# Kernel optimization log

Hardware: AMD Instinct MI355X
Metric: run time of the kernel (lower is better)

The kernel has to match this reference:

```python
import jax, jax.numpy as jnp
import numpy as np

N_HEADS = 16
LN_EPS = 1e-5

def _layernorm(x, g, b):
    m = jnp.mean(x, axis=-1, keepdims=True)
    v = jnp.var(x, axis=-1, keepdims=True)
    return (x - m) * jax.lax.rsqrt(v + LN_EPS) * g + b

def setup_inputs() -> dict:
    key = jax.random.key(0)
    ks = jax.random.split(key, 6)
    B, L, D = 4, 1024, 1024
    Dff = 4 * D
    s = 0.02  # init scale to keep logits/activations in a sane range
    return {
        "X": jax.random.normal(ks[0], (B, L, D), jnp.float32),
        "wq": jax.random.normal(ks[1], (D, D), jnp.float32) * s,
        "wk": jax.random.normal(ks[2], (D, D), jnp.float32) * s,
        "wv": jax.random.normal(ks[3], (D, D), jnp.float32) * s,
        "ln1_g": jnp.ones((D,), jnp.float32),
        "ln1_b": jnp.zeros((D,), jnp.float32),
        "w1": jax.random.normal(ks[4], (Dff, D), jnp.float32) * s,
        "b1": jnp.zeros((Dff,), jnp.float32),
        "w2": jax.random.normal(ks[5], (D, Dff), jnp.float32) * s,
        "b2": jnp.zeros((D,), jnp.float32),
        "ln2_g": jnp.ones((D,), jnp.float32),
        "ln2_b": jnp.zeros((D,), jnp.float32),
    }

def reference(X, wq, wk, wv, ln1_g, ln1_b, w1, b1, w2, b2, ln2_g, ln2_b):
    B, L, D = X.shape
    H = N_HEADS
    dh = D // H
    # qkv projections (torch Linear: x @ W^T), split into heads
    Q = (X @ wq.T).reshape(B, L, H, dh)
    K = (X @ wk.T).reshape(B, L, H, dh)
    V = (X @ wv.T).reshape(B, L, H, dh)
    scores = jnp.einsum("blhd,bmhd->bhlm", Q, K)  # [B,H,L,L]
    causal = jnp.tril(jnp.ones((L, L), dtype=bool))
    scores = jnp.where(causal, scores, -jnp.inf)
    attn = jax.nn.softmax(scores / jnp.sqrt(jnp.asarray(dh, X.dtype)), axis=-1)
    ctx = jnp.einsum("bhlm,bmhd->blhd", attn, V).reshape(B, L, D)
    # post-LN residual (note: no output projection after attention)
    X = _layernorm(X + ctx, ln1_g, ln1_b)
    h = jax.nn.selu(X @ w1.T + b1)
    X = _layernorm(X + h @ w2.T + b2, ln2_g, ln2_b)
    return X
```

## Files before the change

kernel.cpp:

```cpp
#include <hip/hip_runtime.h>
#include <hip/hip_bf16.h>

#define BATCH 4
#define SEQ   1024
#define DIM   1024
#define NH    16
#define DH    64
#define DFF   4096
#define MTOK  (BATCH*SEQ)

#define QSCALE 0.1803368801111204f

typedef __attribute__((ext_vector_type(8))) short  short8;
typedef __attribute__((ext_vector_type(4))) short  short4v;
typedef __attribute__((ext_vector_type(4))) float  floatx4;
typedef __attribute__((ext_vector_type(4))) float  float4v;
typedef __attribute__((ext_vector_type(4))) int    int4v;

__device__ inline float bf2f(short s) {
    return __uint_as_float(((unsigned int)(unsigned short)s) << 16);
}
__device__ inline short f2bf(float f) {
    __hip_bfloat16 h = __float2bfloat16(f);
    return *reinterpret_cast<short*>(&h);
}

__device__ inline float wave_sum(float v) {
    #pragma unroll
    for (int off = 32; off >= 1; off >>= 1) v += __shfl_xor(v, off);
    return v;
}

__device__ inline void async_ld16(short* lds, const short* g) {
    __builtin_amdgcn_global_load_lds(
        (const __attribute__((address_space(1))) void*)g,
        (__attribute__((address_space(3))) void*)lds, 16, 0, 0);
}

#define GBAR() do { asm volatile("" ::: "memory");            \
                    __builtin_amdgcn_s_barrier();             \
                    asm volatile("" ::: "memory"); } while (0)

__global__ __launch_bounds__(256) void convert_all(
    const float* __restrict__ sX,  short* __restrict__ dX,
    const float* __restrict__ sq,  short* __restrict__ dq,
    const float* __restrict__ sk,  short* __restrict__ dk,
    const float* __restrict__ sv,  short* __restrict__ dv,
    const float* __restrict__ s1,  short* __restrict__ d1,
    const float* __restrict__ s2,  short* __restrict__ d2)
{
    int cid = blockIdx.x * 256 + threadIdx.x;
    const float* src; short* dst; int base;
    if      (cid <  524288) { src = sX; dst = dX; base = 0; }
    else if (cid <  655360) { src = sq; dst = dq; base = 524288; }
    else if (cid <  786432) { src = sk; dst = dk; base = 655360; }
    else if (cid <  917504) { src = sv; dst = dv; base = 786432; }
    else if (cid < 1441792) { src = s1; dst = d1; base = 917504; }
    else                    { src = s2; dst = d2; base = 1441792; }
    size_t i = (size_t)(cid - base) * 8;
    float4v f0 = *(const float4v*)(src + i);
    float4v f1 = *(const float4v*)(src + i + 4);
    short8 o;
    o[0]=f2bf(f0[0]); o[1]=f2bf(f0[1]); o[2]=f2bf(f0[2]); o[3]=f2bf(f0[3]);
    o[4]=f2bf(f1[0]); o[5]=f2bf(f1[1]); o[6]=f2bf(f1[2]); o[7]=f2bf(f1[3]);
    *(short8*)(dst + i) = o;
}

template<int EPI>
__global__ __launch_bounds__(512, 2) void gemm256(
    const short* __restrict__ A, const short* __restrict__ B,
    const float* __restrict__ bias, short* __restrict__ C, int N, int K)
{
    __shared__ __align__(16) short Ls[65536];

    const int t    = threadIdx.x;
    const int lane = t & 63;
    const int wave = t >> 6;
    const int quad = lane >> 4;
    const int l15  = lane & 15;
    const int wm   = wave >> 2;
    const int wn   = wave & 3;

    const int nwg2 = gridDim.x * gridDim.y;
    const int lin  = blockIdx.y * gridDim.x + blockIdx.x;
    const int qch  = nwg2 >> 3;
    const int swzb = (lin & 7) * qch + (lin >> 3);
    const int tm   = (swzb % gridDim.x) * 256;
    const int tn   = (swzb / gridDim.x) * 256;

    int kbase = 0, klen = K;
    if (EPI == 3) { klen = K >> 2; kbase = blockIdx.z * klen; }
    const int NT = klen >> 6;

    const int r0 = t >> 3;
    const int rb = ((t >> 8) & 1) * 64 + ((t >> 3) & 31);
    const int g8 = (((t & 7) ^ ((t >> 3) & 7)) << 3);
    const int offAL[2] = { r0*K + g8,          (128 + r0)*K + g8 };
    const int offAH[2] = { (64 + r0)*K + g8,   (192 + r0)*K + g8 };
    const int offB0[2] = { rb*K + g8,          (128 + rb)*K + g8 };
    const int offB1[2] = { (32 + rb)*K + g8,   (160 + rb)*K + g8 };
    const short* Abase = A + (size_t)tm * K + kbase;
    const short* Bbase = B + (size_t)tn * K + kbase;
    short* dstb = &Ls[t * 8];

    const int xa  = (wm*64 + l15) * 64;
    const int xb  = (wn*32 + l15) * 64;
    const int sw  = l15 & 7;
    const int xc0 = ((quad ^ sw) << 3);
    const int xc1 = (((4 + quad) ^ sw) << 3);

    short8 a[4][2], b[4][2];
    floatx4 acc[8][4];
    #pragma unroll
    for (int mt = 0; mt < 8; mt++)
        #pragma unroll
        for (int nt = 0; nt < 4; nt++) acc[mt][nt] = {0.f, 0.f, 0.f, 0.f};

#define STAGE(buf, slot, offs, base, k0) do {                         \
        short* _d = dstb + (buf)*32768 + (slot)*8192;                 \
        async_ld16(_d,        (base) + (offs)[0] + (k0));             \
        async_ld16(_d + 4096, (base) + (offs)[1] + (k0));             \
    } while (0)

#define LDA4(buf, hf) do { _Pragma("unroll")                          \
    for (int _mt = 0; _mt < 4; _mt++) {                               \
        a[_mt][0] = *(const short8*)&Ls[(buf)*32768 + (hf)*8192 + xa + _mt*1024 + xc0]; \
        a[_mt][1] = *(const short8*)&Ls[(buf)*32768 + (hf)*8192 + xa + _mt*1024 + xc1]; \
    } } while (0)

#define LDB2(buf, bh, o) do { _Pragma("unroll")                       \
    for (int _nn = 0; _nn < 2; _nn++) {                               \
        b[(o)+_nn][0] = *(const short8*)&Ls[(buf)*32768 + 16384 + (bh)*8192 + xb + _nn*1024 + xc0]; \
        b[(o)+_nn][1] = *(const short8*)&Ls[(buf)*32768 + 16384 + (bh)*8192 + xb + _nn*1024 + xc1]; \
    } } while (0)

#define MM8(mb, nb) do { __builtin_amdgcn_s_setprio(1); _Pragma("unroll") \
    for (int _mt = 0; _mt < 4; _mt++) { _Pragma("unroll")             \
        for (int _nn = 0; _nn < 2; _nn++) {                           \
            acc[(mb)+_mt][(nb)+_nn] = __builtin_amdgcn_mfma_f32_16x16x32_bf16( \
                a[_mt][0], b[(nb)+_nn][0], acc[(mb)+_mt][(nb)+_nn], 0, 0, 0);  \
            acc[(mb)+_mt][(nb)+_nn] = __builtin_amdgcn_mfma_f32_16x16x32_bf16( \
                a[_mt][1], b[(nb)+_nn][1], acc[(mb)+_mt][(nb)+_nn], 0, 0, 0);  \
        } }                                                           \
    __builtin_amdgcn_s_setprio(0); } while (0)

    STAGE(0, 0, offAL, Abase, 0);
    STAGE(0, 2, offB0, Bbase, 0);
    STAGE(0, 3, offB1, Bbase, 0);
    STAGE(0, 1, offAH, Abase, 0);
    asm volatile("s_waitcnt vmcnt(4)" ::: "memory");
    STAGE(1, 0, offAL, Abase, 64);
    STAGE(1, 2, offB0, Bbase, 64);
    STAGE(1, 3, offB1, Bbase, 64);
    asm volatile("s_waitcnt vmcnt(6)" ::: "memory");
    GBAR();

    for (int kt = 0; kt < NT; ++kt) {
        const int  cur = (kt & 1), nxt = cur ^ 1;
        const bool s1  = (kt + 1 < NT);
        const bool s2  = (kt + 2 < NT);
        const int  k1  = (kt + 1) << 6;
        const int  k2  = (kt + 2) << 6;
        LDA4(cur, 0);
        LDB2(cur, 0, 0);
        if (s1) STAGE(nxt, 1, offAH, Abase, k1);
        asm volatile("s_waitcnt lgkmcnt(8)" ::: "memory");
        GBAR(); MM8(0, 0); GBAR();
        LDB2(cur, 1, 2);
        if (s2) STAGE(cur, 0, offAL, Abase, k2);
        GBAR(); MM8(0, 2); GBAR();
        LDA4(cur, 1);
        if (s2) STAGE(cur, 2, offB0, Bbase, k2);
        GBAR(); MM8(4, 0); GBAR();
        if (s2) STAGE(cur, 3, offB1, Bbase, k2);
        if (kt == NT - 2)
            asm volatile("s_waitcnt vmcnt(0)" ::: "memory");
        else if (kt < NT - 2)
            asm volatile("s_waitcnt vmcnt(6)" ::: "memory");
        GBAR(); MM8(4, 2); GBAR();
    }

    const float SS = 1.0507009873554805f;
    const float SA = 1.6732632423543772f;

    #pragma unroll
    for (int mt = 0; mt < 8; mt++) {
        int row0 = tm + wm*128 + (mt >> 2)*64 + (mt & 3)*16 + quad*4;
        #pragma unroll
        for (int nt = 0; nt < 4; nt++) {
            int col = tn + wn*64 + nt*16 + l15;
            if (EPI == 0 && (col >> 10) == 2) {
                int h = (col >> 6) & 15, d = col & 63;
                int bb = row0 >> 10, key = row0 & 1023;
                short4v pv;
                #pragma unroll
                for (int r = 0; r < 4; r++) pv[r] = f2bf(acc[mt][nt][r]);
                *(short4v*)&C[(size_t)2*MTOK*1024
                    + ((size_t)(bb*16 + h)*64 + d)*1024 + key] = pv;
                continue;
            }
            #pragma unroll
            for (int r = 0; r < 4; r++) {
                int row = row0 + r;
                float v = acc[mt][nt][r];
                if (EPI == 0) {
                    int which = col >> 10;
                    if (which == 0) v *= QSCALE;
                    C[(size_t)which * ((size_t)MTOK*1024)
                      + (size_t)row * 1024 + (col & 1023)] = f2bf(v);
                } else if (EPI == 1) {
                    v += bias[col];
                    v = (v > 0.f) ? SS * v
                                  : SS * SA * (exp2f(v * 1.44269504f) - 1.f);
                    C[(size_t)row * N + col] = f2bf(v);
                } else {
                    C[(size_t)blockIdx.z * ((size_t)MTOK*N)
                      + (size_t)row * N + col] = f2bf(v);
                }
            }
        }
    }
#undef STAGE
#undef LDA4
#undef LDB2
#undef MM8
}

__global__ __launch_bounds__(256) void attn_kernel(
    const short* __restrict__ Q, const short* __restrict__ K,
    const short* __restrict__ Vt, short* __restrict__ CTX)
{
    __shared__ __align__(16) short Ks[2][64*64];
    __shared__ __align__(16) short Vs[2][64*64];
    __shared__ __align__(16) short Pl[4][32][72];

    const int t    = threadIdx.x;
    const int lane = t & 63;
    const int wave = t >> 6;
    const int quad = lane >> 4;
    const int l15  = lane & 15;
    const int q0 = (gridDim.x - 1 - blockIdx.x) * 128;
    const int bh = blockIdx.y;
    const int b  = bh >> 4;
    const int h  = bh & 15;

    const size_t headoff = (size_t)b * SEQ * DIM + (size_t)h * DH;
    const short* Qb  = Q + headoff;
    const short* Kb  = K + headoff;
    const short* Vtb = Vt + (size_t)bh * DH * SEQ;

    const int wrow0 = q0 + wave*32;

    short8 aq[2][2];
    #pragma unroll
    for (int mg = 0; mg < 2; mg++)
        #pragma unroll
        for (int c = 0; c < 2; c++)
            aq[mg][c] = *(const short8*)(Qb
                + (size_t)(wrow0 + mg*16 + l15) * DIM + c*32 + quad*8);

    short8 bones;
    {
        short v = (l15 == 0) ? (short)0x3F80 : (short)0;
        #pragma unroll
        for (int e = 0; e < 8; e++) bones[e] = v;
    }

    floatx4 o[2][4], ol[2];
    #pragma unroll
    for (int mg = 0; mg < 2; mg++) {
        #pragma unroll
        for (int nt = 0; nt < 4; nt++) o[mg][nt] = {0.f, 0.f, 0.f, 0.f};
        ol[mg] = {0.f, 0.f, 0.f, 0.f};
    }

    const int swz = (((t & 7) ^ ((t >> 3) & 7))) * 8;
    auto stage = [&](int j0, int sb) {
        #pragma unroll
        for (int p = 0; p < 2; p++) {
            async_ld16(Ks[sb] + (t + p*256)*8,
                       Kb + (size_t)(j0 + (t>>3) + p*32) * DIM + swz);
            async_ld16(Vs[sb] + (t + p*256)*8,
                       Vtb + (size_t)((t>>3) + p*32) * SEQ + j0 + swz);
        }
    };

    const int jend = q0 + 128;
    stage(0, 0);
    __syncthreads();

    int sb = 0;
    for (int j0 = 0; j0 < jend; j0 += 64) {
        if (j0 + 64 < jend) stage(j0 + 64, sb ^ 1);

        if (j0 <= wrow0 + 31) {
            floatx4 s[2][4];
            #pragma unroll
            for (int mg = 0; mg < 2; mg++)
                #pragma unroll
                for (int nt = 0; nt < 4; nt++) s[mg][nt] = {0.f, 0.f, 0.f, 0.f};
            #pragma unroll
            for (int c = 0; c < 2; c++) {
                #pragma unroll
                for (int nt = 0; nt < 4; nt++) {
                    short8 bk = *(const short8*)&Ks[sb][(nt*16 + l15)*64
                                  + ((c*4 + quad) ^ (l15 & 7))*8];
                    s[0][nt] = __builtin_amdgcn_mfma_f32_16x16x32_bf16(bk, aq[0][c], s[0][nt], 0, 0, 0);
                    s[1][nt] = __builtin_amdgcn_mfma_f32_16x16x32_bf16(bk, aq[1][c], s[1][nt], 0, 0, 0);
                }
            }

            if (j0 + 63 > wrow0) {
                #pragma unroll
                for (int mg = 0; mg < 2; mg++) {
                    int rowq = wrow0 + mg*16 + l15;
                    #pragma unroll
                    for (int nt = 0; nt < 4; nt++) {
                        #pragma unroll
                        for (int r = 0; r < 4; r++) {
                            int key = j0 + nt*16 + quad*4 + r;
                            if (key > rowq) s[mg][nt][r] = -1.0e38f;
                        }
                    }
                }
            }

            #pragma unroll
            for (int mg = 0; mg < 2; mg++)
                #pragma unroll
                for (int nt = 0; nt < 4; nt++) {
                    short4v pv;
                    #pragma unroll
                    for (int r = 0; r < 4; r++)
                        pv[r] = f2bf(exp2f(s[mg][nt][r]));
                    *(short4v*)&Pl[wave][mg*16 + l15][nt*16 + quad*4] = pv;
                }

            #pragma unroll
            for (int c = 0; c < 2; c++) {
                short8 ap0 = *(const short8*)&Pl[wave][l15][c*32 + quad*8];
                short8 ap1 = *(const short8*)&Pl[wave][16 + l15][c*32 + quad*8];
                #pragma unroll
                for (int nt = 0; nt < 4; nt++) {
                    short8 bv = *(const short8*)&Vs[sb][(nt*16 + l15)*64
                                  + ((c*4 + quad) ^ (l15 & 7))*8];
                    o[0][nt] = __builtin_amdgcn_mfma_f32_16x16x32_bf16(ap0, bv, o[0][nt], 0, 0, 0);
                    o[1][nt] = __builtin_amdgcn_mfma_f32_16x16x32_bf16(ap1, bv, o[1][nt], 0, 0, 0);
                }
                ol[0] = __builtin_amdgcn_mfma_f32_16x16x32_bf16(ap0, bones, ol[0], 0, 0, 0);
                ol[1] = __builtin_amdgcn_mfma_f32_16x16x32_bf16(ap1, bones, ol[1], 0, 0, 0);
            }
        }

        __syncthreads();
        sb ^= 1;
    }

    #pragma unroll
    for (int mg = 0; mg < 2; mg++) {
        float linv[4];
        #pragma unroll
        for (int r = 0; r < 4; r++)
            linv[r] = 1.f / __shfl(ol[mg][r], lane & 48);
        #pragma unroll
        for (int nt = 0; nt < 4; nt++) {
            #pragma unroll
            for (int r = 0; r < 4; r++) {
                int rowq = wrow0 + mg*16 + quad*4 + r;
                int d    = nt*16 + l15;
                CTX[(size_t)b * SEQ * DIM + (size_t)rowq * DIM + h*DH + d]
                    = f2bf(o[mg][nt][r] * linv[r]);
            }
        }
    }
}

__global__ __launch_bounds__(256) void ln1_kernel(
    const float* __restrict__ X, const short* __restrict__ ctx,
    const float* __restrict__ g, const float* __restrict__ bvec,
    short* __restrict__ out)
{
    __shared__ float red[8];
    const size_t base = (size_t)blockIdx.x * DIM;
    const int wave = threadIdx.x >> 6;

    float x[4];
    float sum = 0.f, sq = 0.f;
    #pragma unroll
    for (int i = 0; i < 4; i++) {
        int idx = threadIdx.x + i*256;
        float v = X[base + idx] + bf2f(ctx[base + idx]);
        x[i] = v; sum += v; sq += v*v;
    }
    sum = wave_sum(sum); sq = wave_sum(sq);
    if ((threadIdx.x & 63) == 0) { red[wave] = sum; red[4 + wave] = sq; }
    __syncthreads();
    float s1 = red[0] + red[1] + red[2] + red[3];
    float s2 = red[4] + red[5] + red[6] + red[7];
    float mean = s1 * (1.f / DIM);
    float var  = s2 * (1.f / DIM) - mean * mean;
    float rstd = rsqrtf(var + 1e-5f);
    #pragma unroll
    for (int i = 0; i < 4; i++) {
        int idx = threadIdx.x + i*256;
        out[base + idx] = f2bf((x[i] - mean) * rstd * g[idx] + bvec[idx]);
    }
}

__global__ __launch_bounds__(256) void ln2_fused(
    const short* __restrict__ P, const float* __restrict__ bias,
    const short* __restrict__ x1, const float* __restrict__ g,
    const float* __restrict__ bvec, float* __restrict__ out)
{
    __shared__ float red[8];
    const size_t base = (size_t)blockIdx.x * DIM;
    const size_t E4 = (size_t)MTOK * 1024;
    const int wave = threadIdx.x >> 6;

    float x[4];
    float sum = 0.f, sq = 0.f;
    #pragma unroll
    for (int i = 0; i < 4; i++) {
        int idx = threadIdx.x + i*256;
        size_t p = base + idx;
        float v = bf2f(P[p]) + bf2f(P[E4 + p]) + bf2f(P[2*E4 + p])
                + bf2f(P[3*E4 + p]) + bias[idx] + bf2f(x1[p]);
        x[i] = v; sum += v; sq += v*v;
    }
    sum = wave_sum(sum); sq = wave_sum(sq);
    if ((threadIdx.x & 63) == 0) { red[wave] = sum; red[4 + wave] = sq; }
    __syncthreads();
    float s1 = red[0] + red[1] + red[2] + red[3];
    float s2 = red[4] + red[5] + red[6] + red[7];
    float mean = s1 * (1.f / DIM);
    float var  = s2 * (1.f / DIM) - mean * mean;
    float rstd = rsqrtf(var + 1e-5f);
    #pragma unroll
    for (int i = 0; i < 4; i++) {
        int idx = threadIdx.x + i*256;
        out[base + idx] = (x[i] - mean) * rstd * g[idx] + bvec[idx];
    }
}

extern "C" void kernel_launch(void* const* d_in, const int* in_sizes, int n_in,
                              void* d_out, int out_size, void* d_ws, size_t ws_size,
                              hipStream_t stream)
{
    const float* X   = (const float*)d_in[0];
    const float* wq  = (const float*)d_in[1];
    const float* wk  = (const float*)d_in[2];
    const float* wv  = (const float*)d_in[3];
    const float* g1  = (const float*)d_in[4];
    const float* b1  = (const float*)d_in[5];
    const float* w1  = (const float*)d_in[6];
    const float* bb1 = (const float*)d_in[7];
    const float* w2  = (const float*)d_in[8];
    const float* bb2 = (const float*)d_in[9];
    const float* g2  = (const float*)d_in[10];
    const float* b2  = (const float*)d_in[11];

    short* ws = (short*)d_ws;
    const size_t E1 = 1048576, E4 = 4194304;
    size_t o = 0;
    short* Xb    = ws + o; o += E4;
    short* wqkvb = ws + o; o += 3*E1;
    short* w1b   = ws + o; o += E4;
    short* w2b   = ws + o; o += E4;
    short* Q     = ws + o; o += E4;
    short* Kb    = ws + o; o += E4;
    short* Vt    = ws + o; o += E4;
    short* CTX   = ws + o; o += E4;
    short* X1    = ws + o; o += E4;
    short* P     = ws + o; o += 4*E4;
    short* Hf    = Q;

    dim3 blk(256);
    convert_all<<<dim3(7680), blk, 0, stream>>>(
        X, Xb, wq, wqkvb, wk, wqkvb + E1, wv, wqkvb + 2*E1,
        w1, w1b, w2, w2b);

    gemm256<0><<<dim3(MTOK/256, 3072/256), dim3(512), 0, stream>>>(
        Xb, wqkvb, nullptr, Q, 3072, DIM);
    attn_kernel<<<dim3(SEQ/128, BATCH*NH), blk, 0, stream>>>(Q, Kb, Vt, CTX);
    ln1_kernel<<<dim3(MTOK), blk, 0, stream>>>(X, CTX, g1, b1, X1);
    gemm256<1><<<dim3(MTOK/256, DFF/256), dim3(512), 0, stream>>>(
        X1, w1b, bb1, Hf, DFF, DIM);
    gemm256<3><<<dim3(MTOK/256, DIM/256, 4), dim3(512), 0, stream>>>(
        Hf, w2b, nullptr, P, DIM, DFF);
    ln2_fused<<<dim3(MTOK), blk, 0, stream>>>(P, bb2, X1, g2, b2, (float*)d_out);
}
```

Measured before the change: 290.7 us.

## Restructure GEMM main loop into two coarse phases and drop block swizzle

The bf16 GEMM inner loop is reorganised. Each iteration now loads all B fragments at once and runs two large MFMA batches (32 MFMAs each) separated by single barriers, instead of four interleaved load/compute/barrier sub-phases. The vmcnt waits are adjusted to match the new staging order. The XCD-aware block-index swizzle is replaced with plain blockIdx mapping. The aim is fewer barriers and waits, at the cost of less fine-grained overlap of LDS reads with MFMA and possibly worse L2 locality across XCDs.

After: 282.5 us. -2.8%, faster.

```diff
diff --git a/kernel.cpp b/kernel.cpp
--- a/kernel.cpp
+++ b/kernel.cpp
@@ -80,13 +80,8 @@
     const int l15  = lane & 15;
     const int wm   = wave >> 2;
     const int wn   = wave & 3;
-
-    const int nwg2 = gridDim.x * gridDim.y;
-    const int lin  = blockIdx.y * gridDim.x + blockIdx.x;
-    const int qch  = nwg2 >> 3;
-    const int swzb = (lin & 7) * qch + (lin >> 3);
-    const int tm   = (swzb % gridDim.x) * 256;
-    const int tn   = (swzb / gridDim.x) * 256;
+    const int tm   = blockIdx.x * 256;
+    const int tn   = blockIdx.y * 256;
 
     int kbase = 0, klen = K;
     if (EPI == 3) { klen = K >> 2; kbase = blockIdx.z * klen; }
@@ -128,56 +123,54 @@
         a[_mt][1] = *(const short8*)&Ls[(buf)*32768 + (hf)*8192 + xa + _mt*1024 + xc1]; \
     } } while (0)
 
-#define LDB2(buf, bh, o) do { _Pragma("unroll")                       \
-    for (int _nn = 0; _nn < 2; _nn++) {                               \
-        b[(o)+_nn][0] = *(const short8*)&Ls[(buf)*32768 + 16384 + (bh)*8192 + xb + _nn*1024 + xc0]; \
-        b[(o)+_nn][1] = *(const short8*)&Ls[(buf)*32768 + 16384 + (bh)*8192 + xb + _nn*1024 + xc1]; \
-    } } while (0)
-
-#define MM8(mb, nb) do { __builtin_amdgcn_s_setprio(1); _Pragma("unroll") \
-    for (int _mt = 0; _mt < 4; _mt++) { _Pragma("unroll")             \
+#define LDB4(buf) do { _Pragma("unroll")                              \
+    for (int _bh = 0; _bh < 2; _bh++) { _Pragma("unroll")             \
         for (int _nn = 0; _nn < 2; _nn++) {                           \
-            acc[(mb)+_mt][(nb)+_nn] = __builtin_amdgcn_mfma_f32_16x16x32_bf16( \
-                a[_mt][0], b[(nb)+_nn][0], acc[(mb)+_mt][(nb)+_nn], 0, 0, 0);  \
-            acc[(mb)+_mt][(nb)+_nn] = __builtin_amdgcn_mfma_f32_16x16x32_bf16( \
-                a[_mt][1], b[(nb)+_nn][1], acc[(mb)+_mt][(nb)+_nn], 0, 0, 0);  \
-        } }                                                           \
+            b[_bh*2+_nn][0] = *(const short8*)&Ls[(buf)*32768 + 16384 + _bh*8192 + xb + _nn*1024 + xc0]; \
+            b[_bh*2+_nn][1] = *(const short8*)&Ls[(buf)*32768 + 16384 + _bh*8192 + xb + _nn*1024 + xc1]; \
+        } } } while (0)
+
+#define MM32(mb) do { __builtin_amdgcn_s_setprio(1); _Pragma("unroll") \
+    for (int _c = 0; _c < 2; _c++) { _Pragma("unroll")                \
+        for (int _mt = 0; _mt < 4; _mt++) { _Pragma("unroll")         \
+            for (int _nn = 0; _nn < 4; _nn++) {                       \
+                acc[(mb)+_mt][_nn] = __builtin_amdgcn_mfma_f32_16x16x32_bf16( \
+                    a[_mt][_c], b[_nn][_c], acc[(mb)+_mt][_nn], 0, 0, 0);     \
+            } } }                                                     \
     __builtin_amdgcn_s_setprio(0); } while (0)
 
     STAGE(0, 0, offAL, Abase, 0);
     STAGE(0, 2, offB0, Bbase, 0);
     STAGE(0, 3, offB1, Bbase, 0);
     STAGE(0, 1, offAH, Abase, 0);
-    asm volatile("s_waitcnt vmcnt(4)" ::: "memory");
     STAGE(1, 0, offAL, Abase, 64);
     STAGE(1, 2, offB0, Bbase, 64);
     STAGE(1, 3, offB1, Bbase, 64);
-    asm volatile("s_waitcnt vmcnt(6)" ::: "memory");
+    asm volatile("s_waitcnt vmcnt(8)" ::: "memory");
     GBAR();
 
     for (int kt = 0; kt < NT; ++kt) {
-        const int  cur = (kt & 1), nxt = cur ^ 1;
-        const bool s1  = (kt + 1 < NT);
-        const bool s2  = (kt + 2 < NT);
-        const int  k1  = (kt + 1) << 6;
-        const int  k2  = (kt + 2) << 6;
+        const int cur = (kt & 1), nxt = cur ^ 1;
         LDA4(cur, 0);
-        LDB2(cur, 0, 0);
-        if (s1) STAGE(nxt, 1, offAH, Abase, k1);
-        asm volatile("s_waitcnt lgkmcnt(8)" ::: "memory");
-        GBAR(); MM8(0, 0); GBAR();
-        LDB2(cur, 1, 2);
-        if (s2) STAGE(cur, 0, offAL, Abase, k2);
-        GBAR(); MM8(0, 2); GBAR();
+        LDB4(cur);
+        if (kt + 1 < NT) STAGE(nxt, 1, offAH, Abase, (kt + 1) << 6);
+        asm volatile("s_waitcnt lgkmcnt(0)" ::: "memory");
+        if (kt < NT - 1) asm volatile("s_waitcnt vmcnt(8)" ::: "memory");
+        else             asm volatile("s_waitcnt vmcnt(0)" ::: "memory");
+        GBAR();
+        MM32(0);
         LDA4(cur, 1);
-        if (s2) STAGE(cur, 2, offB0, Bbase, k2);
-        GBAR(); MM8(4, 0); GBAR();
-        if (s2) STAGE(cur, 3, offB1, Bbase, k2);
-        if (kt == NT - 2)
-            asm volatile("s_waitcnt vmcnt(0)" ::: "memory");
-        else if (kt < NT - 2)
-            asm volatile("s_waitcnt vmcnt(6)" ::: "memory");
-        GBAR(); MM8(4, 2); GBAR();
+        if (kt + 2 < NT) {
+            STAGE(cur, 0, offAL, Abase, (kt + 2) << 6);
+            STAGE(cur, 2, offB0, Bbase, (kt + 2) << 6);
+            STAGE(cur, 3, offB1, Bbase, (kt + 2) << 6);
+        }
+        asm volatile("s_waitcnt lgkmcnt(0)" ::: "memory");
+        if (kt < NT - 2)       asm volatile("s_waitcnt vmcnt(8)" ::: "memory");
+        else if (kt == NT - 2) asm volatile("s_waitcnt vmcnt(2)" ::: "memory");
+        else                   asm volatile("s_waitcnt vmcnt(0)" ::: "memory");
+        GBAR();
+        MM32(4);
     }
 
     const float SS = 1.0507009873554805f;
@@ -222,8 +215,8 @@
     }
 #undef STAGE
 #undef LDA4
-#undef LDB2
-#undef MM8
+#undef LDB4
+#undef MM32
 }
 
 __global__ __launch_bounds__(256) void attn_kernel(
```
